# Kernel tuning notes

Hardware: AMD Instinct MI355X
Metric: run time of the kernel (lower is better)

The kernel has to match this reference:

```python
import math
import jax, jax.numpy as jnp
import numpy as np

B, W, C = 2, 2048, 1024
N, K = 16, 64  # heads, head dim (C // N)


def setup_inputs() -> dict:
    key = jax.random.key(0)
    ks = jax.random.split(key, 6)
    return {
        "in_sequence_bwc": jax.random.normal(ks[0], (B, W, C), dtype=jnp.float32),
        "W_proj": jax.random.normal(ks[1], (C, C), dtype=jnp.float32) * (1.0 / math.sqrt(C)),
        "b_proj": jax.random.normal(ks[2], (C,), dtype=jnp.float32) * 0.01,
        "generators_1nwk": jax.random.normal(ks[3], (1, N, W, K), dtype=jnp.float32),
        "W_mix": jax.random.normal(ks[4], (C, C), dtype=jnp.float32) * (1.0 / math.sqrt(C)),
        "b_mix": jax.random.normal(ks[5], (C,), dtype=jnp.float32) * 0.01,
    }


def reference(in_sequence_bwc, W_proj, b_proj, generators_1nwk, W_mix, b_mix):
    b, w, c = in_sequence_bwc.shape
    # shared projection (torch Linear: x @ W.T + b)
    p_bwc = in_sequence_bwc @ W_proj.T + b_proj
    p_bnwk = p_bwc.reshape(b, w, N, K).transpose(0, 2, 1, 3)  # [b, n, w, k]
    g_nwk = generators_1nwk[0, :, :w, :]  # [n, w, k]
    # data-dependent metric generator: p^T @ G -> [b, n, k, k]
    m_bnkk = jnp.einsum("bnwk,nwl->bnkl", p_bnwk, g_nwk)
    tril_kk = jnp.tril(jnp.ones((K, K), dtype=in_sequence_bwc.dtype))
    m_bnkk = m_bnkk * tril_kk  # lower-triangular mask on k x k
    m_bnkk = m_bnkk @ jnp.swapaxes(m_bnkk, -1, -2)  # PSD metric M M^T
    # bilinear scores: P @ M @ P^T, scaled
    pm_bnwk = jnp.einsum("bnwk,bnkl->bnwl", p_bnwk, m_bnkk)
    scores_bnww = jnp.einsum("bnwk,bnvk->bnwv", pm_bnwk, p_bnwk) / math.sqrt(K)
    causal = jnp.tril(jnp.ones((w, w), dtype=bool))
    scores_bnww = jnp.where(causal, scores_bnww, -jnp.inf)
    attn_bnww = jax.nn.softmax(scores_bnww, axis=-1)
    nudged_bnwk = attn_bnww @ p_bnwk
    nudged_bwc = nudged_bnwk.transpose(0, 2, 1, 3).reshape(b, w, c)
    return nudged_bwc @ W_mix.T + b_mix
```

## Files before the change

kernel.cpp:

```cpp
#include <hip/hip_runtime.h>
#include <math.h>

#define B_  2
#define W_  2048
#define C_  1024
#define NH_ 16
#define KD_ 64

__device__ __forceinline__ int sw(int r, int c) {
    return (r << 6) + ((((c >> 2) ^ ((r >> 2) & 7)) << 2) | (c & 3));
}

__device__ __forceinline__ void stage64s(const float* __restrict__ src,
                                         float* dst, int tid) {
#pragma unroll
    for (int q = 0; q < 4; ++q) {
        int idx = tid + (q << 8);
        int r   = idx >> 4;
        int c   = (idx & 15) << 2;
        *(float4*)&dst[sw(r, c)] = *(const float4*)(src + (idx << 2));
    }
}

__device__ __forceinline__ void stage64(const float* __restrict__ src,
                                        float (*dst)[68], int tid) {
#pragma unroll
    for (int q = 0; q < 4; ++q) {
        int idx = tid + (q << 8);
        int e   = idx << 2;
        int r   = e >> 6;
        int c   = e & 63;
        *(float4*)&dst[r][c] = *(const float4*)(src + e);
    }
}

template<int OUT_P_LAYOUT>
__global__ __launch_bounds__(256, 2)
void gemm_nt(const float* __restrict__ A, const float* __restrict__ Bw,
             const float* __restrict__ bias, float* __restrict__ Cout)
{
    __shared__ float As[16][68];
    __shared__ float Bs[16][68];
    const int tid = threadIdx.x;
    const int tx  = tid & 15, ty = tid >> 4;
    const int m0  = blockIdx.x << 6;
    const int n0  = blockIdx.y << 6;
    const int lrow = tid >> 2;
    const int lkq  = (tid & 3) << 2;
    const float* Ap = A  + (size_t)(m0 + lrow) * C_ + lkq;
    const float* Bp = Bw + (size_t)(n0 + lrow) * C_ + lkq;

    float acc[4][4] = {};
    for (int k0 = 0; k0 < C_; k0 += 16) {
        float4 av = *(const float4*)(Ap + k0);
        float4 bv = *(const float4*)(Bp + k0);
        __syncthreads();
        As[lkq+0][lrow] = av.x; As[lkq+1][lrow] = av.y;
        As[lkq+2][lrow] = av.z; As[lkq+3][lrow] = av.w;
        Bs[lkq+0][lrow] = bv.x; Bs[lkq+1][lrow] = bv.y;
        Bs[lkq+2][lrow] = bv.z; Bs[lkq+3][lrow] = bv.w;
        __syncthreads();
#pragma unroll
        for (int kk = 0; kk < 16; ++kk) {
            float4 a4 = *(const float4*)&As[kk][ty << 2];
            float4 b4 = *(const float4*)&Bs[kk][tx << 2];
            float am[4] = {a4.x, a4.y, a4.z, a4.w};
            float bm[4] = {b4.x, b4.y, b4.z, b4.w};
#pragma unroll
            for (int i = 0; i < 4; ++i)
#pragma unroll
                for (int j = 0; j < 4; ++j)
                    acc[i][j] = fmaf(am[i], bm[j], acc[i][j]);
        }
    }

    const int gc = n0 + (tx << 2);
    float4 bb = *(const float4*)&bias[gc];
#pragma unroll
    for (int i = 0; i < 4; ++i) {
        int gm = m0 + (ty << 2) + i;
        float4 o;
        o.x = acc[i][0] + bb.x;
        o.y = acc[i][1] + bb.y;
        o.z = acc[i][2] + bb.z;
        o.w = acc[i][3] + bb.w;
        if (OUT_P_LAYOUT) {
            int b = gm >> 11;
            int w = gm & 2047;
            int n = gc >> 6;
            int k = gc & 63;
            *(float4*)(Cout + (((size_t)(b * NH_ + n) * W_ + w) * KD_ + k)) = o;
        } else {
            *(float4*)(Cout + (size_t)gm * C_ + gc) = o;
        }
    }
}

__global__ __launch_bounds__(256, 2)
void metric_part(const float* __restrict__ p, const float* __restrict__ g,
                 float* __restrict__ part)
{
    __shared__ float Ps[32][68];
    __shared__ float Gs[32][68];
    const int ch  = blockIdx.x;
    const int bn  = blockIdx.y;
    const int n   = bn & (NH_ - 1);
    const int tid = threadIdx.x;
    const int tx  = tid & 15, ty = tid >> 4;
    const float* pb = p + (size_t)bn * W_ * KD_ + (size_t)(ch << 8) * KD_;
    const float* gb = g + (size_t)n  * W_ * KD_ + (size_t)(ch << 8) * KD_;

    float acc[4][4] = {};
    for (int w0 = 0; w0 < 256; w0 += 32) {
        __syncthreads();
#pragma unroll
        for (int q = 0; q < 2; ++q) {
            int idx = tid + (q << 8);
            int e   = idx << 2;
            int r   = e >> 6;
            int c   = e & 63;
            *(float4*)&Ps[r][c] = *(const float4*)(pb + (size_t)(w0 + r) * KD_ + c);
            *(float4*)&Gs[r][c] = *(const float4*)(gb + (size_t)(w0 + r) * KD_ + c);
        }
        __syncthreads();
#pragma unroll 8
        for (int w = 0; w < 32; ++w) {
            float4 a4 = *(const float4*)&Ps[w][ty << 2];
            float4 b4 = *(const float4*)&Gs[w][tx << 2];
            float am[4] = {a4.x, a4.y, a4.z, a4.w};
            float bm[4] = {b4.x, b4.y, b4.z, b4.w};
#pragma unroll
            for (int i = 0; i < 4; ++i)
#pragma unroll
                for (int j = 0; j < 4; ++j)
                    acc[i][j] = fmaf(am[i], bm[j], acc[i][j]);
        }
    }

    float* ob = part + (size_t)(bn * 8 + ch) * KD_ * KD_;
#pragma unroll
    for (int i = 0; i < 4; ++i) {
        float4 o; o.x = acc[i][0]; o.y = acc[i][1]; o.z = acc[i][2]; o.w = acc[i][3];
        *(float4*)(ob + ((ty << 2) + i) * KD_ + (tx << 2)) = o;
    }
}

__global__ __launch_bounds__(256, 2)
void metric_reduce(const float* __restrict__ part, float* __restrict__ m2)
{
    __shared__ float M1s[64][68];
    const int bn  = blockIdx.x;
    const int tid = threadIdx.x;
    const int tx  = tid & 15, ty = tid >> 4;
    const float* pb = part + (size_t)bn * 8 * KD_ * KD_;

#pragma unroll
    for (int v = 0; v < 4; ++v) {
        int f = tid + (v << 8);
        int e = f << 2;
        float4 s = *(const float4*)(pb + e);
#pragma unroll
        for (int c = 1; c < 8; ++c) {
            float4 t = *(const float4*)(pb + c * 4096 + e);
            s.x += t.x; s.y += t.y; s.z += t.z; s.w += t.w;
        }
        int k = e >> 6, l = e & 63;
        if (l + 0 > k) s.x = 0.f;
        if (l + 1 > k) s.y = 0.f;
        if (l + 2 > k) s.z = 0.f;
        if (l + 3 > k) s.w = 0.f;
        *(float4*)&M1s[k][l] = s;
    }
    __syncthreads();

    float a2[4][4] = {};
#pragma unroll
    for (int jq = 0; jq < 64; jq += 4) {
        float4 av[4], bv[4];
#pragma unroll
        for (int i = 0; i < 4; ++i) av[i] = *(const float4*)&M1s[(ty << 2) + i][jq];
#pragma unroll
        for (int j = 0; j < 4; ++j) bv[j] = *(const float4*)&M1s[(tx << 2) + j][jq];
#pragma unroll
        for (int i = 0; i < 4; ++i)
#pragma unroll
            for (int j = 0; j < 4; ++j)
                a2[i][j] += av[i].x * bv[j].x + av[i].y * bv[j].y +
                            av[i].z * bv[j].z + av[i].w * bv[j].w;
    }

    float* ob = m2 + (size_t)bn * KD_ * KD_;
#pragma unroll
    for (int i = 0; i < 4; ++i) {
        float4 o; o.x = a2[i][0]; o.y = a2[i][1]; o.z = a2[i][2]; o.w = a2[i][3];
        *(float4*)(ob + ((ty << 2) + i) * KD_ + (tx << 2)) = o;
    }
}

__global__ __launch_bounds__(256, 2)
void qgen_k(const float* __restrict__ p, const float* __restrict__ m2,
            float* __restrict__ qout)
{
    __shared__ float Pt[64][68];
    __shared__ float Ms[64][68];
    const int bn  = blockIdx.y;
    const int w0  = blockIdx.x << 6;
    const int tid = threadIdx.x;
    const int tx  = tid & 15, ty = tid >> 4;
    const float* pb = p  + (size_t)bn * W_ * KD_ + (size_t)w0 * KD_;
    const float* mb = m2 + (size_t)bn * KD_ * KD_;

    stage64(pb, Pt, tid);
    stage64(mb, Ms, tid);
    __syncthreads();

    float acc[4][4] = {};
#pragma unroll
    for (int kq = 0; kq < 64; kq += 4) {
        float4 av[4];
        float  bm[4][4];
#pragma unroll
        for (int i = 0; i < 4; ++i) av[i] = *(const float4*)&Pt[(ty << 2) + i][kq];
#pragma unroll
        for (int kk = 0; kk < 4; ++kk) {
            float4 t = *(const float4*)&Ms[kq + kk][tx << 2];
            bm[kk][0] = t.x; bm[kk][1] = t.y; bm[kk][2] = t.z; bm[kk][3] = t.w;
        }
#pragma unroll
        for (int i = 0; i < 4; ++i) {
            float am[4] = {av[i].x, av[i].y, av[i].z, av[i].w};
#pragma unroll
            for (int j = 0; j < 4; ++j)
                acc[i][j] = fmaf(am[0], bm[0][j],
                            fmaf(am[1], bm[1][j],
                            fmaf(am[2], bm[2][j],
                            fmaf(am[3], bm[3][j], acc[i][j]))));
        }
    }

    float* ob = qout + (size_t)bn * W_ * KD_ + (size_t)w0 * KD_;
#pragma unroll
    for (int i = 0; i < 4; ++i) {
        float4 o;
        o.x = acc[i][0] * 0.125f; o.y = acc[i][1] * 0.125f;
        o.z = acc[i][2] * 0.125f; o.w = acc[i][3] * 0.125f;
        *(float4*)(ob + ((ty << 2) + i) * KD_ + (tx << 2)) = o;
    }
}

__global__ __launch_bounds__(256, 2)
void attn_k(const float* __restrict__ qg, const float* __restrict__ p,
            float* __restrict__ nud)
{
    __shared__ float Qs[4096];
    __shared__ float Ks[4096];
    __shared__ float Es[4096];
    const int bid = blockIdx.x;
    const int bn  = bid & 31;
    const int qt  = 31 - (bid >> 5);
    const int b   = bn >> 4, n = bn & 15;
    const int tid = threadIdx.x;
    const int tx  = tid & 15, ty = tid >> 4;
    const float* qb = qg + (size_t)bn * W_ * KD_ + (size_t)(qt << 6) * KD_;
    const float* kb = p  + (size_t)bn * W_ * KD_;

    stage64s(qb, Qs, tid);

    float acc[4][4] = {};
    float mi[4], li[4];
#pragma unroll
    for (int i = 0; i < 4; ++i) { mi[i] = -INFINITY; li[i] = 0.f; }

    for (int j0 = 0; j0 <= qt; ++j0) {
        __syncthreads();
        stage64s(kb + (size_t)(j0 << 6) * KD_, Ks, tid);
        __syncthreads();

        float s[4][4] = {};
#pragma unroll
        for (int kq = 0; kq < 64; kq += 4) {
            float4 av[4], bv[4];
#pragma unroll
            for (int i = 0; i < 4; ++i) av[i] = *(const float4*)&Qs[sw((ty << 2) + i, kq)];
#pragma unroll
            for (int j = 0; j < 4; ++j) bv[j] = *(const float4*)&Ks[sw((tx << 2) + j, kq)];
#pragma unroll
            for (int i = 0; i < 4; ++i)
#pragma unroll
                for (int j = 0; j < 4; ++j)
                    s[i][j] = fmaf(av[i].x, bv[j].x,
                              fmaf(av[i].y, bv[j].y,
                              fmaf(av[i].z, bv[j].z,
                              fmaf(av[i].w, bv[j].w, s[i][j]))));
        }

        if (j0 == qt) {
#pragma unroll
            for (int i = 0; i < 4; ++i)
#pragma unroll
                for (int j = 0; j < 4; ++j)
                    if (((tx << 2) + j) > ((ty << 2) + i)) s[i][j] = -INFINITY;
        }

        float mnew[4], al[4];
#pragma unroll
        for (int i = 0; i < 4; ++i) {
            float rm = fmaxf(fmaxf(s[i][0], s[i][1]), fmaxf(s[i][2], s[i][3]));
            rm = fmaxf(rm, __shfl_xor(rm, 1, 16));
            rm = fmaxf(rm, __shfl_xor(rm, 2, 16));
            rm = fmaxf(rm, __shfl_xor(rm, 4, 16));
            rm = fmaxf(rm, __shfl_xor(rm, 8, 16));
            mnew[i] = fmaxf(mi[i], rm);
        }
#pragma unroll
        for (int i = 0; i < 4; ++i) {
#pragma unroll
            for (int j = 0; j < 4; ++j) s[i][j] = __expf(s[i][j] - mnew[i]);
            float rs = s[i][0] + s[i][1] + s[i][2] + s[i][3];
            rs += __shfl_xor(rs, 1, 16);
            rs += __shfl_xor(rs, 2, 16);
            rs += __shfl_xor(rs, 4, 16);
            rs += __shfl_xor(rs, 8, 16);
            al[i] = __expf(mi[i] - mnew[i]);
            li[i] = li[i] * al[i] + rs;
            mi[i] = mnew[i];
        }
#pragma unroll
        for (int i = 0; i < 4; ++i) {
            float4 e; e.x = s[i][0]; e.y = s[i][1]; e.z = s[i][2]; e.w = s[i][3];
            *(float4*)&Es[sw((ty << 2) + i, tx << 2)] = e;
#pragma unroll
            for (int j = 0; j < 4; ++j) acc[i][j] *= al[i];
        }
        __syncthreads();

#pragma unroll
        for (int jq = 0; jq < 64; jq += 4) {
            float4 av[4];
            float  vm[4][4];
#pragma unroll
            for (int i = 0; i < 4; ++i) av[i] = *(const float4*)&Es[sw((ty << 2) + i, jq)];
#pragma unroll
            for (int kk = 0; kk < 4; ++kk) {
                float4 t = *(const float4*)&Ks[sw(jq + kk, tx << 2)];
                vm[kk][0] = t.x; vm[kk][1] = t.y; vm[kk][2] = t.z; vm[kk][3] = t.w;
            }
#pragma unroll
            for (int i = 0; i < 4; ++i) {
                float am[4] = {av[i].x, av[i].y, av[i].z, av[i].w};
#pragma unroll
                for (int c = 0; c < 4; ++c)
                    acc[i][c] = fmaf(am[0], vm[0][c],
                                fmaf(am[1], vm[1][c],
                                fmaf(am[2], vm[2][c],
                                fmaf(am[3], vm[3][c], acc[i][c]))));
            }
        }
    }

    const int wrow = qt << 6;
#pragma unroll
    for (int i = 0; i < 4; ++i) {
        float inv = 1.f / li[i];
        float4 o;
        o.x = acc[i][0] * inv; o.y = acc[i][1] * inv;
        o.z = acc[i][2] * inv; o.w = acc[i][3] * inv;
        size_t row = (size_t)(b * W_ + wrow + (ty << 2) + i);
        *(float4*)(nud + row * C_ + (n << 6) + (tx << 2)) = o;
    }
}

extern "C" void kernel_launch(void* const* d_in, const int* in_sizes, int n_in,
                              void* d_out, int out_size, void* d_ws, size_t ws_size,
                              hipStream_t stream)
{
    (void)in_sizes; (void)n_in; (void)out_size; (void)ws_size;
    const float* X  = (const float*)d_in[0];
    const float* Wp = (const float*)d_in[1];
    const float* bp = (const float*)d_in[2];
    const float* G  = (const float*)d_in[3];
    const float* Wm = (const float*)d_in[4];
    const float* bm = (const float*)d_in[5];
    float* out = (float*)d_out;
    float* ws  = (float*)d_ws;

    float* Pbuf = ws;
    float* Qbuf = ws + 4194304;
    float* M2   = ws + 8388608;
    float* Nud  = ws + 8519680;
    float* Part = Qbuf;

    dim3 blk(256);
    gemm_nt<1>   <<<dim3(64, 16), blk, 0, stream>>>(X, Wp, bp, Pbuf);
    metric_part  <<<dim3(8, 32),  blk, 0, stream>>>(Pbuf, G, Part);
    metric_reduce<<<dim3(32),     blk, 0, stream>>>(Part, M2);
    qgen_k       <<<dim3(32, 32), blk, 0, stream>>>(Pbuf, M2, Qbuf);
    attn_k       <<<dim3(1024),   blk, 0, stream>>>(Qbuf, Pbuf, Nud);
    gemm_nt<0>   <<<dim3(64, 16), blk, 0, stream>>>(Nud, Wm, bm, out);
}
```

Baseline: 842.6 us.

## Split long causal attention rows into KV chunks with a combine pass

The causal attention kernel now splits query tiles with many key blocks into up to three chunks of at most 12 key blocks each. Tiles 0-11 stay whole, tiles 12-23 get two chunks and tiles 24-31 get three, giving 1920 blocks in place of 1024. Split chunks write unnormalised partial outputs plus row max and sum to a workspace, and a new combine kernel merges them with log-sum-exp rescaling. The aim is to even out per-block work and shorten the tail set by the longest query tiles, at the cost of an extra launch, partial-buffer traffic, and falling back to the old path when the workspace is too small.

```diff
diff --git a/kernel.cpp b/kernel.cpp
--- a/kernel.cpp
+++ b/kernel.cpp
@@ -7,30 +7,15 @@
 #define NH_ 16
 #define KD_ 64
 
-__device__ __forceinline__ int sw(int r, int c) {
+__device__ __forceinline__ int swz2(int r, int c) {
     return (r << 6) + ((((c >> 2) ^ ((r >> 2) & 7)) << 2) | (c & 3));
 }
-
-__device__ __forceinline__ void stage64s(const float* __restrict__ src,
-                                         float* dst, int tid) {
-#pragma unroll
-    for (int q = 0; q < 4; ++q) {
-        int idx = tid + (q << 8);
-        int r   = idx >> 4;
-        int c   = (idx & 15) << 2;
-        *(float4*)&dst[sw(r, c)] = *(const float4*)(src + (idx << 2));
-    }
-}
-
-__device__ __forceinline__ void stage64(const float* __restrict__ src,
-                                        float (*dst)[68], int tid) {
-#pragma unroll
-    for (int q = 0; q < 4; ++q) {
-        int idx = tid + (q << 8);
-        int e   = idx << 2;
-        int r   = e >> 6;
-        int c   = e & 63;
-        *(float4*)&dst[r][c] = *(const float4*)(src + e);
+__device__ __forceinline__ void stage_sw2(const float* __restrict__ src,
+                                          float* dst, int tid, int nf4) {
+    for (int idx = tid; idx < nf4; idx += 256) {
+        int r = idx >> 4;
+        int c = (idx & 15) << 2;
+        *(float4*)&dst[swz2(r, c)] = *(const float4*)(src + (idx << 2));
     }
 }
 
@@ -210,8 +195,15 @@
     const float* pb = p  + (size_t)bn * W_ * KD_ + (size_t)w0 * KD_;
     const float* mb = m2 + (size_t)bn * KD_ * KD_;
 
-    stage64(pb, Pt, tid);
-    stage64(mb, Ms, tid);
+#pragma unroll
+    for (int q = 0; q < 4; ++q) {
+        int idx = tid + (q << 8);
+        int e   = idx << 2;
+        int r   = e >> 6;
+        int c   = e & 63;
+        *(float4*)&Pt[r][c] = *(const float4*)(pb + e);
+        *(float4*)&Ms[r][c] = *(const float4*)(mb + e);
+    }
     __syncthreads();
 
     float acc[4][4] = {};
@@ -249,31 +241,45 @@
 }
 
 __global__ __launch_bounds__(256, 2)
-void attn_k(const float* __restrict__ qg, const float* __restrict__ p,
-            float* __restrict__ nud)
+void attn_ck(const float* __restrict__ qg, const float* __restrict__ p,
+             float* __restrict__ nud, float* __restrict__ part, int mode)
 {
     __shared__ float Qs[4096];
     __shared__ float Ks[4096];
     __shared__ float Es[4096];
     const int bid = blockIdx.x;
     const int bn  = bid & 31;
-    const int qt  = 31 - (bid >> 5);
     const int b   = bn >> 4, n = bn & 15;
     const int tid = threadIdx.x;
     const int tx  = tid & 15, ty = tid >> 4;
-    const float* qb = qg + (size_t)bn * W_ * KD_ + (size_t)(qt << 6) * KD_;
-    const float* kb = p  + (size_t)bn * W_ * KD_;
-
-    stage64s(qb, Qs, tid);
+
+    int qt, js, je, direct, slot = 0;
+    if (mode == 0) {
+        int cid = bid >> 5;
+        qt = 31 - cid; js = 0; je = qt + 1; direct = 1;
+    } else {
+        int cid = 59 - (bid >> 5);
+        int c0;
+        if (cid < 12)      { qt = cid;                c0 = 0; }
+        else if (cid < 36) { qt = 12 + ((cid-12)>>1); c0 = (cid-12)&1; }
+        else               { qt = 24 + (cid-36)/3;    c0 = (cid-36)%3; }
+        js = c0 * 12;
+        je = min(js + 12, qt + 1);
+        direct = (qt < 12);
+        slot = bn * 60 + cid;
+    }
+
+    const float* pb = p + (size_t)bn * W_ * KD_;
+    stage_sw2(qg + (size_t)bn * W_ * KD_ + (size_t)(qt << 6) * KD_, Qs, tid, 1024);
 
     float acc[4][4] = {};
     float mi[4], li[4];
 #pragma unroll
     for (int i = 0; i < 4; ++i) { mi[i] = -INFINITY; li[i] = 0.f; }
 
-    for (int j0 = 0; j0 <= qt; ++j0) {
-        __syncthreads();
-        stage64s(kb + (size_t)(j0 << 6) * KD_, Ks, tid);
+    for (int j0 = js; j0 < je; ++j0) {
+        __syncthreads();
+        stage_sw2(pb + (size_t)(j0 << 6) * KD_, Ks, tid, 1024);
         __syncthreads();
 
         float s[4][4] = {};
@@ -281,9 +287,9 @@
         for (int kq = 0; kq < 64; kq += 4) {
             float4 av[4], bv[4];
 #pragma unroll
-            for (int i = 0; i < 4; ++i) av[i] = *(const float4*)&Qs[sw((ty << 2) + i, kq)];
-#pragma unroll
-            for (int j = 0; j < 4; ++j) bv[j] = *(const float4*)&Ks[sw((tx << 2) + j, kq)];
+            for (int i = 0; i < 4; ++i) av[i] = *(const float4*)&Qs[swz2((ty << 2) + i, kq)];
+#pragma unroll
+            for (int j = 0; j < 4; ++j) bv[j] = *(const float4*)&Ks[swz2((tx << 2) + j, kq)];
 #pragma unroll
             for (int i = 0; i < 4; ++i)
 #pragma unroll
@@ -302,7 +308,6 @@
                     if (((tx << 2) + j) > ((ty << 2) + i)) s[i][j] = -INFINITY;
         }
 
-        float mnew[4], al[4];
 #pragma unroll
         for (int i = 0; i < 4; ++i) {
             float rm = fmaxf(fmaxf(s[i][0], s[i][1]), fmaxf(s[i][2], s[i][3]));
@@ -310,63 +315,103 @@
             rm = fmaxf(rm, __shfl_xor(rm, 2, 16));
             rm = fmaxf(rm, __shfl_xor(rm, 4, 16));
             rm = fmaxf(rm, __shfl_xor(rm, 8, 16));
-            mnew[i] = fmaxf(mi[i], rm);
-        }
-#pragma unroll
-        for (int i = 0; i < 4; ++i) {
-#pragma unroll
-            for (int j = 0; j < 4; ++j) s[i][j] = __expf(s[i][j] - mnew[i]);
+            float mnew = fmaxf(mi[i], rm);
+#pragma unroll
+            for (int j = 0; j < 4; ++j) s[i][j] = __expf(s[i][j] - mnew);
             float rs = s[i][0] + s[i][1] + s[i][2] + s[i][3];
             rs += __shfl_xor(rs, 1, 16);
             rs += __shfl_xor(rs, 2, 16);
             rs += __shfl_xor(rs, 4, 16);
             rs += __shfl_xor(rs, 8, 16);
-            al[i] = __expf(mi[i] - mnew[i]);
-            li[i] = li[i] * al[i] + rs;
-            mi[i] = mnew[i];
-        }
+            float al = __expf(mi[i] - mnew);
+            li[i] = li[i] * al + rs;
+            mi[i] = mnew;
+            float4 e; e.x = s[i][0]; e.y = s[i][1]; e.z = s[i][2]; e.w = s[i][3];
+            *(float4*)&Es[swz2((ty << 2) + i, tx << 2)] = e;
+#pragma unroll
+            for (int j = 0; j < 4; ++j) acc[i][j] *= al;
+        }
+        __syncthreads();
+
+#pragma unroll
+        for (int jq = 0; jq < 64; jq += 4) {
+            float4 vm[4];
+#pragma unroll
+            for (int kk = 0; kk < 4; ++kk) vm[kk] = *(const float4*)&Ks[swz2(jq + kk, tx << 2)];
+#pragma unroll
+            for (int i = 0; i < 4; ++i) {
+                float4 a = *(const float4*)&Es[swz2((ty << 2) + i, jq)];
+                acc[i][0] = fmaf(a.x, vm[0].x, fmaf(a.y, vm[1].x,
+                            fmaf(a.z, vm[2].x, fmaf(a.w, vm[3].x, acc[i][0]))));
+                acc[i][1] = fmaf(a.x, vm[0].y, fmaf(a.y, vm[1].y,
+                            fmaf(a.z, vm[2].y, fmaf(a.w, vm[3].y, acc[i][1]))));
+                acc[i][2] = fmaf(a.x, vm[0].z, fmaf(a.y, vm[1].z,
+                            fmaf(a.z, vm[2].z, fmaf(a.w, vm[3].z, acc[i][2]))));
+                acc[i][3] = fmaf(a.x, vm[0].w, fmaf(a.y, vm[1].w,
+                            fmaf(a.z, vm[2].w, fmaf(a.w, vm[3].w, acc[i][3]))));
+            }
+        }
+    }
+
+    if (direct) {
+        const int wrow = qt << 6;
 #pragma unroll
         for (int i = 0; i < 4; ++i) {
-            float4 e; e.x = s[i][0]; e.y = s[i][1]; e.z = s[i][2]; e.w = s[i][3];
-            *(float4*)&Es[sw((ty << 2) + i, tx << 2)] = e;
-#pragma unroll
-            for (int j = 0; j < 4; ++j) acc[i][j] *= al[i];
-        }
-        __syncthreads();
-
-#pragma unroll
-        for (int jq = 0; jq < 64; jq += 4) {
-            float4 av[4];
-            float  vm[4][4];
-#pragma unroll
-            for (int i = 0; i < 4; ++i) av[i] = *(const float4*)&Es[sw((ty << 2) + i, jq)];
-#pragma unroll
-            for (int kk = 0; kk < 4; ++kk) {
-                float4 t = *(const float4*)&Ks[sw(jq + kk, tx << 2)];
-                vm[kk][0] = t.x; vm[kk][1] = t.y; vm[kk][2] = t.z; vm[kk][3] = t.w;
+            float inv = 1.f / li[i];
+            float4 o;
+            o.x = acc[i][0] * inv; o.y = acc[i][1] * inv;
+            o.z = acc[i][2] * inv; o.w = acc[i][3] * inv;
+            size_t row = (size_t)(b * W_ + wrow + (ty << 2) + i);
+            *(float4*)(nud + row * C_ + (n << 6) + (tx << 2)) = o;
+        }
+    } else {
+        float* ob = part + (size_t)slot * 4224;
+#pragma unroll
+        for (int i = 0; i < 4; ++i) {
+            int r = (ty << 2) + i;
+            float4 o;
+            o.x = acc[i][0]; o.y = acc[i][1]; o.z = acc[i][2]; o.w = acc[i][3];
+            *(float4*)(ob + (r << 6) + (tx << 2)) = o;
+            if (tx == 0) {
+                ob[4096 + r] = mi[i];
+                ob[4160 + r] = li[i];
             }
-#pragma unroll
-            for (int i = 0; i < 4; ++i) {
-                float am[4] = {av[i].x, av[i].y, av[i].z, av[i].w};
-#pragma unroll
-                for (int c = 0; c < 4; ++c)
-                    acc[i][c] = fmaf(am[0], vm[0][c],
-                                fmaf(am[1], vm[1][c],
-                                fmaf(am[2], vm[2][c],
-                                fmaf(am[3], vm[3][c], acc[i][c]))));
-            }
-        }
-    }
-
-    const int wrow = qt << 6;
-#pragma unroll
-    for (int i = 0; i < 4; ++i) {
-        float inv = 1.f / li[i];
-        float4 o;
-        o.x = acc[i][0] * inv; o.y = acc[i][1] * inv;
-        o.z = acc[i][2] * inv; o.w = acc[i][3] * inv;
-        size_t row = (size_t)(b * W_ + wrow + (ty << 2) + i);
-        *(float4*)(nud + row * C_ + (n << 6) + (tx << 2)) = o;
+        }
+    }
+}
+
+__global__ __launch_bounds__(256, 2)
+void combine_k(const float* __restrict__ part, float* __restrict__ nud)
+{
+    const int bid = blockIdx.x;
+    const int bn  = bid & 31;
+    const int qt  = 12 + (bid >> 5);
+    const int b   = bn >> 4, n = bn & 15;
+    int nc, cid0;
+    if (qt < 24) { nc = 2; cid0 = 12 + ((qt - 12) << 1); }
+    else         { nc = 3; cid0 = 36 + 3 * (qt - 24); }
+    const float* p0 = part + (size_t)(bn * 60 + cid0) * 4224;
+    const int tid = threadIdx.x;
+
+#pragma unroll
+    for (int k = 0; k < 4; ++k) {
+        int f4 = tid + (k << 8);
+        int e  = f4 << 2;
+        int r  = e >> 6;
+        float M = -INFINITY;
+        for (int c = 0; c < nc; ++c)
+            M = fmaxf(M, p0[c * 4224 + 4096 + r]);
+        float Ox = 0.f, Oy = 0.f, Oz = 0.f, Ow = 0.f, L = 0.f;
+        for (int c = 0; c < nc; ++c) {
+            float w = __expf(p0[c * 4224 + 4096 + r] - M);
+            float4 t = *(const float4*)(p0 + c * 4224 + e);
+            Ox += w * t.x; Oy += w * t.y; Oz += w * t.z; Ow += w * t.w;
+            L  += w * p0[c * 4224 + 4160 + r];
+        }
+        float inv = 1.f / L;
+        float4 o; o.x = Ox * inv; o.y = Oy * inv; o.z = Oz * inv; o.w = Ow * inv;
+        size_t row = (size_t)(b * W_ + (qt << 6) + r);
+        *(float4*)(nud + row * C_ + (n << 6) + (e & 63)) = o;
     }
 }
 
@@ -374,7 +419,7 @@
                               void* d_out, int out_size, void* d_ws, size_t ws_size,
                               hipStream_t stream)
 {
-    (void)in_sizes; (void)n_in; (void)out_size; (void)ws_size;
+    (void)in_sizes; (void)n_in; (void)out_size;
     const float* X  = (const float*)d_in[0];
     const float* Wp = (const float*)d_in[1];
     const float* bp = (const float*)d_in[2];
@@ -384,17 +429,26 @@
     float* out = (float*)d_out;
     float* ws  = (float*)d_ws;
 
-    float* Pbuf = ws;
-    float* Qbuf = ws + 4194304;
-    float* M2   = ws + 8388608;
-    float* Nud  = ws + 8519680;
-    float* Part = Qbuf;
+    float* Pbuf  = ws;
+    float* Qbuf  = ws + 4194304;
+    float* M2    = ws + 8388608;
+    float* Nud   = ws + 8519680;
+    float* Part2 = ws + 12713984;
+
+    const size_t needF = 12713984ULL + 1920ULL * 4224ULL;
+    const bool big = ws_size >= needF * sizeof(float);
+    float* MPart = big ? Part2 : Nud;
 
     dim3 blk(256);
     gemm_nt<1>   <<<dim3(64, 16), blk, 0, stream>>>(X, Wp, bp, Pbuf);
-    metric_part  <<<dim3(8, 32),  blk, 0, stream>>>(Pbuf, G, Part);
-    metric_reduce<<<dim3(32),     blk, 0, stream>>>(Part, M2);
+    metric_part  <<<dim3(8, 32),  blk, 0, stream>>>(Pbuf, G, MPart);
+    metric_reduce<<<dim3(32),     blk, 0, stream>>>(MPart, M2);
     qgen_k       <<<dim3(32, 32), blk, 0, stream>>>(Pbuf, M2, Qbuf);
-    attn_k       <<<dim3(1024),   blk, 0, stream>>>(Qbuf, Pbuf, Nud);
+    if (big) {
+        attn_ck  <<<dim3(1920),   blk, 0, stream>>>(Qbuf, Pbuf, Nud, Part2, 1);
+        combine_k<<<dim3(640),    blk, 0, stream>>>(Part2, Nud);
+    } else {
+        attn_ck  <<<dim3(1024),   blk, 0, stream>>>(Qbuf, Pbuf, Nud, Part2, 0);
+    }
     gemm_nt<0>   <<<dim3(64, 16), blk, 0, stream>>>(Nud, Wm, bm, out);
 }
```

After: 978.7 us. +16.2%, slower.
